# Optimization experiments

Hardware: AMD Instinct MI355X
Metric: run time of the kernel (lower is better)

## Reference

```python
import jax, jax.numpy as jnp
import numpy as np

DIM = 1024
NUM_HEADS = 16
HEAD_DIM = DIM // NUM_HEADS
SCALE = HEAD_DIM ** -0.5


def setup_inputs() -> dict:
    key = jax.random.key(0)
    k1, k2, k3 = jax.random.split(key, 3)
    B, N = 2, 2048
    x = jax.random.normal(k1, (B, N, DIM), dtype=jnp.float32)
    # qkv: Linear(dim, 3*dim, bias=False); proj: Linear(dim, dim) with bias
    w_qkv = jax.random.normal(k2, (3 * DIM, DIM), dtype=jnp.float32) * (DIM ** -0.5)
    w_proj = jax.random.normal(k3, (DIM, DIM), dtype=jnp.float32) * (DIM ** -0.5)
    b_proj = jnp.zeros((DIM,), dtype=jnp.float32)
    return {"x": x, "w_qkv": w_qkv, "w_proj": w_proj, "b_proj": b_proj}


def reference(x, w_qkv, w_proj, b_proj):
    B, N, C = x.shape
    H, D = NUM_HEADS, HEAD_DIM
    qkv = jnp.einsum('bnc,fc->bnf', x, w_qkv)                 # [B,N,3C]
    qkv = qkv.reshape(B, N, 3, H, D).transpose(2, 0, 3, 1, 4)  # [3,B,H,N,D]
    q, k, v = qkv[0], qkv[1], qkv[2]
    q = q * SCALE
    attn = jnp.einsum('bhnd,bhmd->bhnm', q, k)                 # [B,H,N,N]
    attn = jax.nn.softmax(attn, axis=-1)
    out = jnp.einsum('bhnm,bhmd->bhnd', attn, v)               # [B,H,N,D]
    out = out.transpose(0, 2, 1, 3).reshape(B, N, C)
    out = jnp.einsum('bnc,fc->bnf', out, w_proj) + b_proj
    return out
```

## Files before the change

kernel.cpp:

```cpp
#include <hip/hip_runtime.h>
#include <hip/hip_bf16.h>
#include <stdint.h>

typedef __attribute__((ext_vector_type(4))) float f32x4;
typedef __attribute__((ext_vector_type(16))) float f32x16;
typedef __attribute__((ext_vector_type(8))) short bf16x8;
typedef __attribute__((ext_vector_type(4))) short bf16x4;
typedef unsigned short ushort_t;

#define QSCALE 0.18033688f

__device__ inline short f2bf(float f) {
  unsigned u = __builtin_bit_cast(unsigned, f);
  u += 0x7fffu + ((u >> 16) & 1u);
  return (short)(u >> 16);
}

__device__ inline void gload_lds16(const void* g, void* l) {
  __builtin_amdgcn_global_load_lds(
      (const __attribute__((address_space(1))) void*)g,
      (__attribute__((address_space(3))) void*)l, 16, 0, 0);
}

__device__ inline unsigned cvtpk(float a, float b) {
  unsigned r;
  asm("v_cvt_pk_bf16_f32 %0, %1, %2" : "=v"(r) : "v"(a), "v"(b));
  return r;
}

__device__ inline void swap32u(unsigned& a, unsigned& b) {
  asm("v_permlane32_swap_b32 %0, %1" : "+v"(a), "+v"(b));
}

__global__ __launch_bounds__(256) void cvt_all(const float* __restrict__ x,
                                               const float* __restrict__ wq,
                                               const float* __restrict__ wp,
                                               short* __restrict__ Xb,
                                               short* __restrict__ Wq,
                                               short* __restrict__ Wp) {
  int i = blockIdx.x * 256 + threadIdx.x;
  const float* s;
  short* d;
  int off;
  if (i < 524288)       { s = x;  d = Xb; off = i; }
  else if (i < 917504)  { s = wq; d = Wq; off = i - 524288; }
  else                  { s = wp; d = Wp; off = i - 917504; }
  const float4* sv = (const float4*)s;
  float4 a = sv[2 * off], b = sv[2 * off + 1];
  bf16x8 o;
  o[0] = f2bf(a.x); o[1] = f2bf(a.y); o[2] = f2bf(a.z); o[3] = f2bf(a.w);
  o[4] = f2bf(b.x); o[5] = f2bf(b.y); o[6] = f2bf(b.z); o[7] = f2bf(b.w);
  ((bf16x8*)d)[off] = o;
}

template <int F32OUT, int SPLITV, int BXPX>
__global__ __launch_bounds__(256, 2) void gemm_db(const short* __restrict__ A,
                                                  const short* __restrict__ B,
                                                  void* __restrict__ Cv,
                                                  short* __restrict__ Vtg,
                                                  const float* __restrict__ bias,
                                                  int scale_cols, float scale_val,
                                                  int M, int N, int K) {
  __shared__ char smem[65536];
  short* Ab0 = (short*)smem;
  short* Bb0 = (short*)(smem + 32768);
  const int tid = threadIdx.x, wv = tid >> 6, ln = tid & 63;
  const int wm = wv >> 1, wn = wv & 1;
  const int id = blockIdx.x;
  const int xcd = id & 7, local = id >> 3;
  const int bx = xcd * BXPX + local % BXPX;
  const int by = local / BXPX;
  const int bn0 = bx * 128, bm0 = by * 128;
  const int nt = K >> 6;

  const int srow = ln >> 3;
  const int scol = ((ln & 7) ^ (ln >> 3)) * 8;
  const int fln = ln & 15;
  const int fk = ln >> 4;

  f32x4 acc[4][4] = {};

  auto stage = [&](int t, int s) {
    const size_t k0 = (size_t)t << 6;
#pragma unroll
    for (int rd = 0; rd < 4; rd++) {
      const int ch = 4 * wv + rd;
      gload_lds16(A + (size_t)(bm0 + ch * 8 + srow) * K + k0 + scol,
                  (char*)(Ab0 + s * 8192) + ch * 1024);
      gload_lds16(B + (size_t)(bn0 + ch * 8 + srow) * K + k0 + scol,
                  (char*)(Bb0 + s * 8192) + ch * 1024);
    }
  };

  stage(0, 0);
  stage(1, 1);
  asm volatile("s_waitcnt vmcnt(8)" ::: "memory");
  __builtin_amdgcn_s_barrier();
  __builtin_amdgcn_sched_barrier(0);

  for (int t = 0; t < nt; t++) {
    const int s = t & 1;
    const char* Ap = (const char*)(Ab0 + s * 8192);
    const char* Bp = (const char*)(Bb0 + s * 8192);

    bf16x8 af[4][2], bf[4][2];
#pragma unroll
    for (int m = 0; m < 4; m++) {
      const int R = wm * 64 + m * 16 + fln;
#pragma unroll
      for (int kk = 0; kk < 2; kk++)
        af[m][kk] = *(const bf16x8*)(Ap + R * 128 + ((((kk << 2) | fk) ^ (R & 7)) << 4));
    }
#pragma unroll
    for (int n = 0; n < 4; n++) {
      const int R = wn * 64 + n * 16 + fln;
#pragma unroll
      for (int kk = 0; kk < 2; kk++)
        bf[n][kk] = *(const bf16x8*)(Bp + R * 128 + ((((kk << 2) | fk) ^ (R & 7)) << 4));
    }

    __builtin_amdgcn_s_setprio(1);
#pragma unroll
    for (int kk = 0; kk < 2; kk++)
#pragma unroll
      for (int m = 0; m < 4; m++)
#pragma unroll
        for (int n = 0; n < 4; n++)
          acc[m][n] = __builtin_amdgcn_mfma_f32_16x16x32_bf16(af[m][kk], bf[n][kk], acc[m][n], 0, 0, 0);
    __builtin_amdgcn_s_setprio(0);

    if (t + 1 < nt) {
      __builtin_amdgcn_s_barrier();
      if (t + 2 < nt) {
        stage(t + 2, s);
        asm volatile("s_waitcnt vmcnt(8)" ::: "memory");
      } else {
        asm volatile("s_waitcnt vmcnt(0)" ::: "memory");
      }
      __builtin_amdgcn_s_barrier();
      __builtin_amdgcn_sched_barrier(0);
    }
  }

  if constexpr (SPLITV) {
    if (bn0 >= 2048) {
      __syncthreads();
      short* Vl = (short*)smem;
#pragma unroll
      for (int m = 0; m < 4; m++) {
        const int tok0 = wm * 64 + m * 16 + fk * 4;
#pragma unroll
        for (int n = 0; n < 4; n++) {
          const int f_loc = wn * 64 + n * 16 + fln;
          bf16x4 w;
#pragma unroll
          for (int j = 0; j < 4; j++) w[j] = f2bf(acc[m][n][j]);
          *(bf16x4*)(Vl + f_loc * 136 + tok0) = w;
        }
      }
      __syncthreads();
      const int fbase = bn0 - 2048, bb = bm0 >> 11, ntok0 = bm0 & 2047;
#pragma unroll
      for (int pass = 0; pass < 8; pass++) {
        const int f_loc = wv * 32 + pass * 4 + (ln >> 4);
        const int f = fbase + f_loc;
        const int g = (bb * 16 + (f >> 6)) * 64 + (f & 63);
        bf16x8 w = *(const bf16x8*)(Vl + f_loc * 136 + (ln & 15) * 8);
        *(bf16x8*)(Vtg + (size_t)g * 2048 + ntok0 + (ln & 15) * 8) = w;
      }
      return;
    }
  }

  const int r0 = bm0 + wm * 64, c0 = bn0 + wn * 64;
  const int fg4 = fk * 4;
#pragma unroll
  for (int m = 0; m < 4; m++) {
    const int row0 = r0 + m * 16 + fg4;
#pragma unroll
    for (int n = 0; n < 4; n++) {
      const int col = c0 + n * 16 + fln;
      if constexpr (SPLITV) {
        const float sc = (col < scale_cols) ? scale_val : 1.0f;
#pragma unroll
        for (int j = 0; j < 4; j++)
          ((short*)Cv)[(size_t)(row0 + j) * 2048 + col] = f2bf(acc[m][n][j] * sc);
      } else {
#pragma unroll
        for (int j = 0; j < 4; j++) {
          float v = acc[m][n][j];
          if (col < scale_cols) v *= scale_val;
          if (F32OUT) ((float*)Cv)[(size_t)(row0 + j) * N + col] = v + bias[col];
          else        ((short*)Cv)[(size_t)(row0 + j) * N + col] = f2bf(v);
        }
      }
    }
  }
}

__global__ __launch_bounds__(256, 2) void attn_fwd(const short* __restrict__ QK,
                                                   const short* __restrict__ Vtg,
                                                   short* __restrict__ AO) {
  __shared__ short Ks[3][64 * 64];
  __shared__ short Vt[3][64 * 64];
  const int tid = threadIdx.x, wv = tid >> 6, ln = tid & 63;
  const int lq = ln & 31, hi = ln >> 5;
  const int id = blockIdx.x;
  const int c = (id & 7) * 64 + (id >> 3);
  const int qt = c & 15, bh = c >> 4;
  const int b = bh >> 4, h = bh & 15;
  const short* base = QK + (size_t)(b * 2048) * 2048 + h * 64;
  const short* Kg = base + 1024;
  const short* Vg = Vtg + (size_t)bh * 64 * 2048;
  const int qrow = qt * 128 + wv * 32 + lq;

  bf16x8 qf[4];
  {
    const short* Qrow = base + (size_t)qrow * 2048;
#pragma unroll
    for (int ds = 0; ds < 4; ds++)
      qf[ds] = *(const bf16x8*)(Qrow + ds * 16 + hi * 8);
  }

  const int krow = ln >> 3;
  const int kcol = ((ln & 7) ^ (ln >> 3)) * 8;

  float l_run = 0.f;
  f32x16 o0 = {}, o1 = {};

#define STAGE(t, s)                                                              \
  {                                                                              \
    _Pragma("unroll")                                                            \
    for (int rd = 0; rd < 2; rd++) {                                             \
      const int r8 = 16 * wv + 8 * rd + krow;                                    \
      gload_lds16(Kg + (size_t)((t) * 64 + r8) * 2048 + kcol,                    \
                  (char*)Ks[s] + (2 * wv + rd) * 1024);                          \
      gload_lds16(Vg + (size_t)r8 * 2048 + (t) * 64 + kcol,                      \
                  (char*)Vt[s] + (2 * wv + rd) * 1024);                          \
    }                                                                            \
  }

  STAGE(0, 0);
  STAGE(1, 1);

  for (int t = 0; t < 32; t++) {
    const int s = t % 3;
    if (t < 31) asm volatile("s_waitcnt vmcnt(4)" ::: "memory");
    else        asm volatile("s_waitcnt vmcnt(0)" ::: "memory");
    __builtin_amdgcn_s_barrier();
    __builtin_amdgcn_sched_barrier(0);
    if (t + 2 < 32) STAGE(t + 2, (t + 2) % 3);

    f32x16 c0 = {}, c1 = {};
    const char* Kb = (const char*)Ks[s];
    __builtin_amdgcn_s_setprio(1);
#pragma unroll
    for (int ds = 0; ds < 4; ds++) {
      const int cp = (ds * 2 + hi) ^ (lq & 7);
      bf16x8 ka0 = *(const bf16x8*)(Kb + lq * 128 + cp * 16);
      bf16x8 ka1 = *(const bf16x8*)(Kb + (32 + lq) * 128 + cp * 16);
      c0 = __builtin_amdgcn_mfma_f32_32x32x16_bf16(ka0, qf[ds], c0, 0, 0, 0);
      c1 = __builtin_amdgcn_mfma_f32_32x32x16_bf16(ka1, qf[ds], c1, 0, 0, 0);
    }
    __builtin_amdgcn_s_setprio(0);

#pragma unroll
    for (int r = 0; r < 16; r++) c0[r] = __builtin_amdgcn_exp2f(c0[r]);
#pragma unroll
    for (int r = 0; r < 16; r++) c1[r] = __builtin_amdgcn_exp2f(c1[r]);
    {
      float st[8];
#pragma unroll
      for (int r = 0; r < 8; r++)
        st[r] = (c0[2 * r] + c0[2 * r + 1]) + (c1[2 * r] + c1[2 * r + 1]);
#pragma unroll
      for (int r = 0; r < 4; r++) st[r] += st[r + 4];
      l_run += (st[0] + st[1]) + (st[2] + st[3]);
    }

    bf16x8 pa[4];
#pragma unroll
    for (int cs = 0; cs < 2; cs++) {
      const f32x16& p = cs ? c1 : c0;
#pragma unroll
      for (int ksl = 0; ksl < 2; ksl++) {
        unsigned A0 = cvtpk(p[8 * ksl + 0], p[8 * ksl + 1]);
        unsigned A1 = cvtpk(p[8 * ksl + 2], p[8 * ksl + 3]);
        unsigned B0 = cvtpk(p[8 * ksl + 4], p[8 * ksl + 5]);
        unsigned B1 = cvtpk(p[8 * ksl + 6], p[8 * ksl + 7]);
        swap32u(A0, B0);
        swap32u(A1, B1);
        union { unsigned u[4]; bf16x8 v; } tmp;
        tmp.u[0] = A0; tmp.u[1] = A1; tmp.u[2] = B0; tmp.u[3] = B1;
        pa[cs * 2 + ksl] = tmp.v;
      }
    }

    const char* Vb = (const char*)Vt[s];
    __builtin_amdgcn_s_setprio(1);
#pragma unroll
    for (int ks = 0; ks < 4; ks++) {
      const int cp = (ks * 2 + hi) ^ (lq & 7);
      bf16x8 va0 = *(const bf16x8*)(Vb + lq * 128 + cp * 16);
      bf16x8 va1 = *(const bf16x8*)(Vb + (32 + lq) * 128 + cp * 16);
      o0 = __builtin_amdgcn_mfma_f32_32x32x16_bf16(va0, pa[ks], o0, 0, 0, 0);
      o1 = __builtin_amdgcn_mfma_f32_32x32x16_bf16(va1, pa[ks], o1, 0, 0, 0);
    }
    __builtin_amdgcn_s_setprio(0);
  }
#undef STAGE

  l_run += __shfl_xor(l_run, 32);
  const float inv = __builtin_amdgcn_rcpf(l_run);
  short* Arow = AO + ((size_t)(b * 2048) + qrow) * 1024 + h * 64;
#pragma unroll
  for (int dt = 0; dt < 2; dt++) {
    const f32x16& o = dt ? o1 : o0;
#pragma unroll
    for (int g = 0; g < 4; g++) {
      bf16x4 w;
#pragma unroll
      for (int i = 0; i < 4; i++) w[i] = f2bf(o[4 * g + i] * inv);
      *(bf16x4*)(Arow + dt * 32 + 8 * g + 4 * hi) = w;
    }
  }
}

extern "C" void kernel_launch(void* const* d_in, const int* in_sizes, int n_in,
                              void* d_out, int out_size, void* d_ws, size_t ws_size,
                              hipStream_t stream) {
  const float* x = (const float*)d_in[0];
  const float* w_qkv = (const float*)d_in[1];
  const float* w_proj = (const float*)d_in[2];
  const float* b_proj = (const float*)d_in[3];
  float* out = (float*)d_out;

  char* ws = (char*)d_ws;
  short* Xb  = (short*)(ws + 0);
  short* Wq  = (short*)(ws + 8388608);
  short* Wp  = (short*)(ws + 14680064);
  short* QK  = (short*)(ws + 16777216);
  short* Vtg = (short*)(ws + 33554432);
  short* AO  = (short*)(ws + 41943040);

  cvt_all<<<4096, 256, 0, stream>>>(x, w_qkv, w_proj, Xb, Wq, Wp);

  gemm_db<0, 1, 3><<<dim3(768), 256, 0, stream>>>(Xb, Wq, QK, Vtg, nullptr,
                                                  1024, QSCALE, 4096, 3072, 1024);

  attn_fwd<<<dim3(512), 256, 0, stream>>>(QK, Vtg, AO);

  gemm_db<1, 0, 1><<<dim3(256), 256, 0, stream>>>(AO, Wp, out, nullptr, b_proj,
                                                  0, 1.0f, 4096, 1024, 1024);
}
```

Measured before the change: 103.1 us.

## Process 64 query rows per wave in attention, halve grid, double-buffer K/V

Each wave in the attention kernel now handles two 32-row query tiles, so every K and V fragment read from shared memory feeds twice as many MFMAs. The grid shrinks from 512 to 256 blocks, and the 3-stage asynchronous K/V pipeline with explicit vmcnt waits is replaced by a 2-stage double buffer synchronised with __syncthreads. The aim is more reuse of LDS data and higher MFMA density per load. In exchange, register pressure roughly doubles for accumulators, only 256 blocks may underfill the 256 CUs at 2 waves/SIMD, and the simpler pipeline with full barriers may expose more load latency.

Measured after the change: 108.6 us. 1.05x slower.

```diff
diff --git a/kernel.cpp b/kernel.cpp
--- a/kernel.cpp
+++ b/kernel.cpp
@@ -201,32 +201,35 @@
 __global__ __launch_bounds__(256, 2) void attn_fwd(const short* __restrict__ QK,
                                                    const short* __restrict__ Vtg,
                                                    short* __restrict__ AO) {
-  __shared__ short Ks[3][64 * 64];
-  __shared__ short Vt[3][64 * 64];
+  __shared__ short Ks[2][64 * 64];
+  __shared__ short Vt[2][64 * 64];
   const int tid = threadIdx.x, wv = tid >> 6, ln = tid & 63;
   const int lq = ln & 31, hi = ln >> 5;
   const int id = blockIdx.x;
-  const int c = (id & 7) * 64 + (id >> 3);
-  const int qt = c & 15, bh = c >> 4;
+  const int c = (id & 7) * 32 + (id >> 3);
+  const int qt = c & 7, bh = c >> 3;
   const int b = bh >> 4, h = bh & 15;
   const short* base = QK + (size_t)(b * 2048) * 2048 + h * 64;
   const short* Kg = base + 1024;
   const short* Vg = Vtg + (size_t)bh * 64 * 2048;
-  const int qrow = qt * 128 + wv * 32 + lq;
-
-  bf16x8 qf[4];
+  const int qrowA = qt * 256 + wv * 64 + lq;
+
+  bf16x8 qfA[4], qfB[4];
   {
-    const short* Qrow = base + (size_t)qrow * 2048;
-#pragma unroll
-    for (int ds = 0; ds < 4; ds++)
-      qf[ds] = *(const bf16x8*)(Qrow + ds * 16 + hi * 8);
+    const short* QrA = base + (size_t)qrowA * 2048;
+    const short* QrB = QrA + 32 * 2048;
+#pragma unroll
+    for (int ds = 0; ds < 4; ds++) {
+      qfA[ds] = *(const bf16x8*)(QrA + ds * 16 + hi * 8);
+      qfB[ds] = *(const bf16x8*)(QrB + ds * 16 + hi * 8);
+    }
   }
 
   const int krow = ln >> 3;
   const int kcol = ((ln & 7) ^ (ln >> 3)) * 8;
 
-  float l_run = 0.f;
-  f32x16 o0 = {}, o1 = {};
+  float lA = 0.f, lB = 0.f;
+  f32x16 oA0 = {}, oA1 = {}, oB0 = {}, oB1 = {};
 
 #define STAGE(t, s)                                                              \
   {                                                                              \
@@ -241,17 +244,13 @@
   }
 
   STAGE(0, 0);
-  STAGE(1, 1);
+  __syncthreads();
 
   for (int t = 0; t < 32; t++) {
-    const int s = t % 3;
-    if (t < 31) asm volatile("s_waitcnt vmcnt(4)" ::: "memory");
-    else        asm volatile("s_waitcnt vmcnt(0)" ::: "memory");
-    __builtin_amdgcn_s_barrier();
-    __builtin_amdgcn_sched_barrier(0);
-    if (t + 2 < 32) STAGE(t + 2, (t + 2) % 3);
-
-    f32x16 c0 = {}, c1 = {};
+    const int s = t & 1;
+    if (t < 31) STAGE(t + 1, s ^ 1);
+
+    f32x16 cA0 = {}, cA1 = {}, cB0 = {}, cB1 = {};
     const char* Kb = (const char*)Ks[s];
     __builtin_amdgcn_s_setprio(1);
 #pragma unroll
@@ -259,40 +258,63 @@
       const int cp = (ds * 2 + hi) ^ (lq & 7);
       bf16x8 ka0 = *(const bf16x8*)(Kb + lq * 128 + cp * 16);
       bf16x8 ka1 = *(const bf16x8*)(Kb + (32 + lq) * 128 + cp * 16);
-      c0 = __builtin_amdgcn_mfma_f32_32x32x16_bf16(ka0, qf[ds], c0, 0, 0, 0);
-      c1 = __builtin_amdgcn_mfma_f32_32x32x16_bf16(ka1, qf[ds], c1, 0, 0, 0);
+      cA0 = __builtin_amdgcn_mfma_f32_32x32x16_bf16(ka0, qfA[ds], cA0, 0, 0, 0);
+      cB0 = __builtin_amdgcn_mfma_f32_32x32x16_bf16(ka0, qfB[ds], cB0, 0, 0, 0);
+      cA1 = __builtin_amdgcn_mfma_f32_32x32x16_bf16(ka1, qfA[ds], cA1, 0, 0, 0);
+      cB1 = __builtin_amdgcn_mfma_f32_32x32x16_bf16(ka1, qfB[ds], cB1, 0, 0, 0);
     }
     __builtin_amdgcn_s_setprio(0);
 
 #pragma unroll
-    for (int r = 0; r < 16; r++) c0[r] = __builtin_amdgcn_exp2f(c0[r]);
-#pragma unroll
-    for (int r = 0; r < 16; r++) c1[r] = __builtin_amdgcn_exp2f(c1[r]);
+    for (int r = 0; r < 16; r++) cA0[r] = __builtin_amdgcn_exp2f(cA0[r]);
+#pragma unroll
+    for (int r = 0; r < 16; r++) cA1[r] = __builtin_amdgcn_exp2f(cA1[r]);
+#pragma unroll
+    for (int r = 0; r < 16; r++) cB0[r] = __builtin_amdgcn_exp2f(cB0[r]);
+#pragma unroll
+    for (int r = 0; r < 16; r++) cB1[r] = __builtin_amdgcn_exp2f(cB1[r]);
     {
-      float st[8];
-#pragma unroll
-      for (int r = 0; r < 8; r++)
-        st[r] = (c0[2 * r] + c0[2 * r + 1]) + (c1[2 * r] + c1[2 * r + 1]);
-#pragma unroll
-      for (int r = 0; r < 4; r++) st[r] += st[r + 4];
-      l_run += (st[0] + st[1]) + (st[2] + st[3]);
-    }
-
-    bf16x8 pa[4];
+      float sa[8], sb[8];
+#pragma unroll
+      for (int r = 0; r < 8; r++) {
+        sa[r] = (cA0[2 * r] + cA0[2 * r + 1]) + (cA1[2 * r] + cA1[2 * r + 1]);
+        sb[r] = (cB0[2 * r] + cB0[2 * r + 1]) + (cB1[2 * r] + cB1[2 * r + 1]);
+      }
+#pragma unroll
+      for (int r = 0; r < 4; r++) { sa[r] += sa[r + 4]; sb[r] += sb[r + 4]; }
+      lA += (sa[0] + sa[1]) + (sa[2] + sa[3]);
+      lB += (sb[0] + sb[1]) + (sb[2] + sb[3]);
+    }
+
+    bf16x8 paA[4], paB[4];
 #pragma unroll
     for (int cs = 0; cs < 2; cs++) {
-      const f32x16& p = cs ? c1 : c0;
+      const f32x16& pA = cs ? cA1 : cA0;
+      const f32x16& pB = cs ? cB1 : cB0;
 #pragma unroll
       for (int ksl = 0; ksl < 2; ksl++) {
-        unsigned A0 = cvtpk(p[8 * ksl + 0], p[8 * ksl + 1]);
-        unsigned A1 = cvtpk(p[8 * ksl + 2], p[8 * ksl + 3]);
-        unsigned B0 = cvtpk(p[8 * ksl + 4], p[8 * ksl + 5]);
-        unsigned B1 = cvtpk(p[8 * ksl + 6], p[8 * ksl + 7]);
-        swap32u(A0, B0);
-        swap32u(A1, B1);
-        union { unsigned u[4]; bf16x8 v; } tmp;
-        tmp.u[0] = A0; tmp.u[1] = A1; tmp.u[2] = B0; tmp.u[3] = B1;
-        pa[cs * 2 + ksl] = tmp.v;
+        {
+          unsigned A0 = cvtpk(pA[8 * ksl + 0], pA[8 * ksl + 1]);
+          unsigned A1 = cvtpk(pA[8 * ksl + 2], pA[8 * ksl + 3]);
+          unsigned B0 = cvtpk(pA[8 * ksl + 4], pA[8 * ksl + 5]);
+          unsigned B1 = cvtpk(pA[8 * ksl + 6], pA[8 * ksl + 7]);
+          swap32u(A0, B0);
+          swap32u(A1, B1);
+          union { unsigned u[4]; bf16x8 v; } tmp;
+          tmp.u[0] = A0; tmp.u[1] = A1; tmp.u[2] = B0; tmp.u[3] = B1;
+          paA[cs * 2 + ksl] = tmp.v;
+        }
+        {
+          unsigned A0 = cvtpk(pB[8 * ksl + 0], pB[8 * ksl + 1]);
+          unsigned A1 = cvtpk(pB[8 * ksl + 2], pB[8 * ksl + 3]);
+          unsigned B0 = cvtpk(pB[8 * ksl + 4], pB[8 * ksl + 5]);
+          unsigned B1 = cvtpk(pB[8 * ksl + 6], pB[8 * ksl + 7]);
+          swap32u(A0, B0);
+          swap32u(A1, B1);
+          union { unsigned u[4]; bf16x8 v; } tmp;
+          tmp.u[0] = A0; tmp.u[1] = A1; tmp.u[2] = B0; tmp.u[3] = B1;
+          paB[cs * 2 + ksl] = tmp.v;
+        }
       }
     }
 
@@ -303,25 +325,37 @@
       const int cp = (ks * 2 + hi) ^ (lq & 7);
       bf16x8 va0 = *(const bf16x8*)(Vb + lq * 128 + cp * 16);
       bf16x8 va1 = *(const bf16x8*)(Vb + (32 + lq) * 128 + cp * 16);
-      o0 = __builtin_amdgcn_mfma_f32_32x32x16_bf16(va0, pa[ks], o0, 0, 0, 0);
-      o1 = __builtin_amdgcn_mfma_f32_32x32x16_bf16(va1, pa[ks], o1, 0, 0, 0);
+      oA0 = __builtin_amdgcn_mfma_f32_32x32x16_bf16(va0, paA[ks], oA0, 0, 0, 0);
+      oB0 = __builtin_amdgcn_mfma_f32_32x32x16_bf16(va0, paB[ks], oB0, 0, 0, 0);
+      oA1 = __builtin_amdgcn_mfma_f32_32x32x16_bf16(va1, paA[ks], oA1, 0, 0, 0);
+      oB1 = __builtin_amdgcn_mfma_f32_32x32x16_bf16(va1, paB[ks], oB1, 0, 0, 0);
     }
     __builtin_amdgcn_s_setprio(0);
+
+    __syncthreads();
   }
 #undef STAGE
 
-  l_run += __shfl_xor(l_run, 32);
-  const float inv = __builtin_amdgcn_rcpf(l_run);
-  short* Arow = AO + ((size_t)(b * 2048) + qrow) * 1024 + h * 64;
+  lA += __shfl_xor(lA, 32);
+  lB += __shfl_xor(lB, 32);
+  const float invA = __builtin_amdgcn_rcpf(lA);
+  const float invB = __builtin_amdgcn_rcpf(lB);
+  short* ArA = AO + ((size_t)(b * 2048) + qrowA) * 1024 + h * 64;
+  short* ArB = ArA + 32 * 1024;
 #pragma unroll
   for (int dt = 0; dt < 2; dt++) {
-    const f32x16& o = dt ? o1 : o0;
+    const f32x16& oa = dt ? oA1 : oA0;
+    const f32x16& ob = dt ? oB1 : oB0;
 #pragma unroll
     for (int g = 0; g < 4; g++) {
-      bf16x4 w;
-#pragma unroll
-      for (int i = 0; i < 4; i++) w[i] = f2bf(o[4 * g + i] * inv);
-      *(bf16x4*)(Arow + dt * 32 + 8 * g + 4 * hi) = w;
+      bf16x4 wa, wb;
+#pragma unroll
+      for (int i = 0; i < 4; i++) {
+        wa[i] = f2bf(oa[4 * g + i] * invA);
+        wb[i] = f2bf(ob[4 * g + i] * invB);
+      }
+      *(bf16x4*)(ArA + dt * 32 + 8 * g + 4 * hi) = wa;
+      *(bf16x4*)(ArB + dt * 32 + 8 * g + 4 * hi) = wb;
     }
   }
 }
@@ -348,7 +382,7 @@
   gemm_db<0, 1, 3><<<dim3(768), 256, 0, stream>>>(Xb, Wq, QK, Vtg, nullptr,
                                                   1024, QSCALE, 4096, 3072, 1024);
 
-  attn_fwd<<<dim3(512), 256, 0, stream>>>(QK, Vtg, AO);
+  attn_fwd<<<dim3(256), 256, 0, stream>>>(QK, Vtg, AO);
 
   gemm_db<1, 0, 1><<<dim3(256), 256, 0, stream>>>(AO, Wp, out, nullptr, b_proj,
                                                   0, 1.0f, 4096, 1024, 1024);
```
